# Optimization experiments

Measured on AMD Instinct MI355X. Metric: run time of the kernel, lower is better.

Reference implementation:

```python
import jax, jax.numpy as jnp
import numpy as np

A = 81          # agents / zones (9x9 grid)
DMAX = 5        # max neighborhood size (self + 4-neighbors)
NGLOB = 48      # global obs block width
HID = 128
B = 16384
LN_EPS = 1e-12  # tf.contrib.layers.layer_norm epsilon
BN_EPS = 1e-3   # tf.contrib.layers.batch_norm epsilon
NEG = -1e30


def _grid_adjacency():
    side = 9
    idx = np.zeros((A, DMAX), np.int32)
    mask = np.zeros((A, DMAX), bool)
    for i in range(A):
        r, c = divmod(i, side)
        nb = [i]
        for dr, dc in ((-1, 0), (1, 0), (0, -1), (0, 1)):
            rr, cc = r + dr, c + dc
            if 0 <= rr < side and 0 <= cc < side:
                nb.append(rr * side + cc)
        idx[i, :len(nb)] = nb
        mask[i, :len(nb)] = True
    return jnp.asarray(idx), jnp.asarray(mask)


def setup_inputs() -> dict:
    key = jax.random.key(0)
    ks = jax.random.split(key, 8)
    neigh_idx, neigh_mask = _grid_adjacency()
    in_dim = 2 * DMAX + NGLOB  # padded local obs width (58)
    s = 0.05
    return {
        "obs": jax.random.normal(ks[0], (B, 210), jnp.float32),
        "neigh_idx": neigh_idx,
        "neigh_mask": neigh_mask,
        "W1": jax.random.normal(ks[1], (A, in_dim, HID), jnp.float32) * s,
        "b1": jnp.zeros((A, HID), jnp.float32),
        "ln1_g": jnp.ones((A, HID), jnp.float32),
        "ln1_b": jnp.zeros((A, HID), jnp.float32),
        "bn1_b": jnp.zeros((A, HID), jnp.float32),
        "W2": jax.random.normal(ks[2], (A, HID, HID), jnp.float32) * s,
        "b2": jnp.zeros((A, HID), jnp.float32),
        "ln2_g": jnp.ones((A, HID), jnp.float32),
        "ln2_b": jnp.zeros((A, HID), jnp.float32),
        "bn2_b": jnp.zeros((A, HID), jnp.float32),
        "Wout": jax.random.normal(ks[3], (A, HID, DMAX), jnp.float32) * s,
        "bout": jnp.zeros((A, DMAX), jnp.float32),
    }


def _layer_norm(x, g, b):
    mu = jnp.mean(x, axis=-1, keepdims=True)
    var = jnp.mean(jnp.square(x - mu), axis=-1, keepdims=True)
    return (x - mu) * jax.lax.rsqrt(var + LN_EPS) * g[:, None, :] + b[:, None, :]


def _batch_norm(x, beta):
    # training-mode batch norm over the batch axis (axis=1), center only (scale=False)
    mu = jnp.mean(x, axis=1, keepdims=True)
    var = jnp.mean(jnp.square(x - mu), axis=1, keepdims=True)
    return (x - mu) * jax.lax.rsqrt(var + BN_EPS) + beta[:, None, :]


def reference(obs, neigh_idx, neigh_mask, W1, b1, ln1_g, ln1_b, bn1_b,
              W2, b2, ln2_g, ln2_b, bn2_b, Wout, bout):
    m = neigh_mask[:, None, :].astype(obs.dtype)          # [A,1,DMAX]
    g1 = obs[:, NGLOB + neigh_idx].transpose(1, 0, 2)      # [A,B,DMAX] zone block 1
    g2 = obs[:, NGLOB + 81 + neigh_idx].transpose(1, 0, 2)  # [A,B,DMAX] zone block 2
    glob = jnp.broadcast_to(obs[None, :, :NGLOB], (A, obs.shape[0], NGLOB))
    x = jnp.concatenate([g1 * m, g2 * m, glob], axis=-1)   # [A,B,58] (padded slots zeroed)

    h = jnp.einsum('abi,aio->abo', x, W1) + b1[:, None, :]
    h = jax.nn.relu(_batch_norm(_layer_norm(h, ln1_g, ln1_b), bn1_b))
    h = jnp.einsum('abi,aio->abo', h, W2) + b2[:, None, :]
    h = jax.nn.relu(_batch_norm(_layer_norm(h, ln2_g, ln2_b), bn2_b))

    logits = jnp.einsum('abi,aid->abd', h, Wout) + bout[:, None, :]  # [A,B,DMAX]
    logits = jnp.where(neigh_mask[:, None, :], logits, NEG)
    p = jax.nn.softmax(logits, axis=-1) * m                # masked softmax over valid neighbors

    oh = jax.nn.one_hot(neigh_idx, A, dtype=p.dtype)       # [A,DMAX,81] scatter map
    out = jnp.einsum('abd,adn->abn', p, oh)                # scatter into fixed 81-vector
    return out.transpose(1, 0, 2)                          # [B,A,81]
```

## Files before the change

kernel.cpp:

```cpp
#include <hip/hip_runtime.h>
#include <stdint.h>
#include <stddef.h>

#define N_AG 81

typedef __bf16 bf16x8 __attribute__((ext_vector_type(8)));
typedef float f32x4 __attribute__((ext_vector_type(4)));
typedef uint32_t u32v4 __attribute__((ext_vector_type(4)));
typedef uint32_t u32v2 __attribute__((ext_vector_type(2)));

#define PB 0
#define PG 128
#define PBT 256

#define SWZ(row, off) ((uint32_t)(off) ^ (((uint32_t)(row) & 7u) << 4))

__device__ __forceinline__ unsigned short b2u(__bf16 h) {
  return __builtin_bit_cast(unsigned short, h);
}

__device__ __forceinline__ f32x4 f4z() { f32x4 v; v[0]=0.f; v[1]=0.f; v[2]=0.f; v[3]=0.f; return v; }

__device__ __forceinline__ bf16x8 ld_frag(const uint8_t* p) {
  u32v4 v = *(const u32v4*)p;
  return __builtin_bit_cast(bf16x8, v);
}

__device__ __forceinline__ f32x4 mfma16(bf16x8 a, bf16x8 b, f32x4 c) {
  return __builtin_amdgcn_mfma_f32_16x16x32_bf16(a, b, c, 0, 0, 0);
}

__device__ __forceinline__ uint8_t* yslot(float* out, int b, int a) {
  size_t base = (size_t)b * 26244 + (size_t)a * 324;
  uint32_t pad = (uint32_t)(64 - (base & 63)) & 63u;
  return (uint8_t*)out + base + pad;
}

__device__ __forceinline__ float wave16_sum(float v) {
  v += __builtin_bit_cast(float, __builtin_amdgcn_update_dpp(0, __builtin_bit_cast(int, v), 0xB1, 0xF, 0xF, true));
  v += __builtin_bit_cast(float, __builtin_amdgcn_update_dpp(0, __builtin_bit_cast(int, v), 0x4E, 0xF, 0xF, true));
  v += __builtin_bit_cast(float, __builtin_amdgcn_update_dpp(0, __builtin_bit_cast(int, v), 0x141, 0xF, 0xF, true));
  v += __builtin_bit_cast(float, __builtin_amdgcn_update_dpp(0, __builtin_bit_cast(int, v), 0x140, 0xF, 0xF, true));
  return v;
}

__device__ __forceinline__ bf16x8 mk_frag(const unsigned short (&us)[8]) {
  u32v4 pk;
  pk[0] = (uint32_t)us[0] | ((uint32_t)us[1] << 16);
  pk[1] = (uint32_t)us[2] | ((uint32_t)us[3] << 16);
  pk[2] = (uint32_t)us[4] | ((uint32_t)us[5] << 16);
  pk[3] = (uint32_t)us[6] | ((uint32_t)us[7] << 16);
  return __builtin_bit_cast(bf16x8, pk);
}

__device__ __forceinline__ bf16x8 bn_frag(u32v4 yv, const f32x4 (&cf)[4]) {
  bf16x8 r;
  #pragma unroll
  for (int j = 0; j < 8; ++j) {
    uint32_t us = (j & 1) ? (yv[j >> 1] >> 16) : (yv[j >> 1] & 0xffffu);
    float f = __builtin_bit_cast(float, us << 16);
    float h = fmaf(f, cf[j >> 1][(j & 1) * 2], cf[j >> 1][(j & 1) * 2 + 1]);
    r[j] = (__bf16)fmaxf(h, 0.f);
  }
  return r;
}

__device__ __forceinline__ void bias_ln(f32x4 (&acc)[8][2], const float* s_par, int g) {
  #pragma unroll
  for (int nf = 0; nf < 2; ++nf) {
    float s = 0.f, qs = 0.f;
    #pragma unroll
    for (int mf = 0; mf < 8; ++mf) {
      #pragma unroll
      for (int rg = 0; rg < 4; ++rg) {
        float tv = acc[mf][nf][rg] + s_par[PB + 16 * mf + 4 * g + rg];
        acc[mf][nf][rg] = tv;
        s += tv;
        qs = fmaf(tv, tv, qs);
      }
    }
    s += __shfl_xor(s, 16);  s += __shfl_xor(s, 32);
    qs += __shfl_xor(qs, 16); qs += __shfl_xor(qs, 32);
    float mu = s * (1.f / 128.f);
    float var = qs * (1.f / 128.f) - mu * mu;
    float rstd = rsqrtf(var + 1e-12f);
    #pragma unroll
    for (int mf = 0; mf < 8; ++mf) {
      #pragma unroll
      for (int rg = 0; rg < 4; ++rg) {
        int o = 16 * mf + 4 * g + rg;
        acc[mf][nf][rg] = (acc[mf][nf][rg] - mu) * rstd * s_par[PG + o] + s_par[PBT + o];
      }
    }
  }
}

__device__ __forceinline__ void stats_lds(const f32x4 (&acc)[8][2],
                                          float (&s_red)[2][4][128],
                                          int wv, int g, int q) {
  #pragma unroll
  for (int mf = 0; mf < 8; ++mf) {
    #pragma unroll
    for (int rg = 0; rg < 4; ++rg) {
      float a0v = acc[mf][0][rg], a1v = acc[mf][1][rg];
      float s = a0v + a1v;
      float qq = fmaf(a0v, a0v, a1v * a1v);
      s = wave16_sum(s);
      qq = wave16_sum(qq);
      if (q == 0) {
        int o = 16 * mf + 4 * g + rg;
        s_red[0][wv][o] += s;
        s_red[1][wv][o] += qq;
      }
    }
  }
}

__device__ __forceinline__ void pack_lds(const f32x4 (&acc)[8][2], uint8_t* s_y,
                                         int wv, int g, int q) {
  #pragma unroll
  for (int nf = 0; nf < 2; ++nf) {
    uint32_t row = 32 * wv + 16 * nf + q;
    #pragma unroll
    for (int mf = 0; mf < 8; ++mf) {
      u32v2 pk;
      pk[0] = (uint32_t)b2u((__bf16)acc[mf][nf][0]) | ((uint32_t)b2u((__bf16)acc[mf][nf][1]) << 16);
      pk[1] = (uint32_t)b2u((__bf16)acc[mf][nf][2]) | ((uint32_t)b2u((__bf16)acc[mf][nf][3]) << 16);
      *(u32v2*)(s_y + row * 256 + SWZ(row, 32 * mf + 8 * g)) = pk;
    }
  }
}

__device__ __forceinline__ void burst_out(const uint8_t* s_y, float* out, int tile, int a, int t) {
  const int row = t >> 1, half = t & 1;
  uint8_t* sp = yslot(out, tile * 128 + row, a) + half * 128;
  #pragma unroll
  for (int j = 0; j < 8; ++j) {
    u32v4 v = *(const u32v4*)(s_y + row * 256 + SWZ(row, half * 128 + 16 * j));
    *(u32v4*)(sp + 16 * j) = v;
  }
}

__device__ __forceinline__ void burst_in(uint8_t* s_y, float* out, int tile, int a, int t) {
  const int row = t >> 1, half = t & 1;
  const uint8_t* sp = yslot(out, tile * 128 + row, a) + half * 128;
  #pragma unroll
  for (int j = 0; j < 8; ++j) {
    u32v4 v = *(const u32v4*)(sp + 16 * j);
    *(u32v4*)(s_y + row * 256 + SWZ(row, half * 128 + 16 * j)) = v;
  }
}

__global__ void prep_w1(const float* __restrict__ W1, uint8_t* __restrict__ w1img) {
  const int a = blockIdx.x, t = threadIdx.x;
  for (int i = t; i < 128 * 64; i += 256) {
    int o = i & 127, kk = i >> 7;
    float v;
    if (kk < 48)      v = W1[((size_t)a * 58 + (10 + kk)) * 128 + o];
    else if (kk < 58) v = W1[((size_t)a * 58 + (kk - 48)) * 128 + o];
    else              v = 0.f;
    uint32_t cb = 2u * kk;
    uint32_t phys = o * 128 + (((cb & ~15u) ^ (((uint32_t)o & 7u) << 4)) | (cb & 15u));
    *(unsigned short*)(w1img + (size_t)a * 16384 + phys) = b2u((__bf16)v);
  }
}

__global__ void prep_w2wo(const float* __restrict__ W2, const float* __restrict__ Wout,
                          uint8_t* __restrict__ w2img, uint8_t* __restrict__ woimg) {
  const int a = blockIdx.x, t = threadIdx.x;
  for (int i = t; i < 128 * 128; i += 256) {
    int o = i & 127, kk = i >> 7;
    float v = W2[((size_t)a * 128 + kk) * 128 + o];
    uint32_t cb = 2u * kk;
    uint32_t phys = o * 256 + (((cb & ~15u) ^ (((uint32_t)o & 7u) << 4)) | (cb & 15u));
    *(unsigned short*)(w2img + (size_t)a * 32768 + phys) = b2u((__bf16)v);
  }
  for (int i = t; i < 16 * 128; i += 256) {
    int k = i & 127, d = i >> 7;
    float v = (d < 5) ? Wout[((size_t)a * 128 + k) * 5 + d] : 0.f;
    uint32_t cb = 2u * k;
    uint32_t phys = d * 256 + (((cb & ~15u) ^ (((uint32_t)d & 7u) << 4)) | (cb & 15u));
    *(unsigned short*)(woimg + (size_t)a * 4096 + phys) = b2u((__bf16)v);
  }
}

__global__ void prep_obs(const float* __restrict__ obs, uint8_t* __restrict__ globimg) {
  const int row = blockIdx.x * 256 + threadIdx.x;
  if (row >= 16384) return;
  const float* orow = obs + (size_t)row * 210;
  uint8_t* dst = globimg + (size_t)row * 96;
  #pragma unroll
  for (int c = 0; c < 6; ++c) {
    u32v4 pk;
    #pragma unroll
    for (int e = 0; e < 4; ++e) {
      pk[e] = (uint32_t)b2u((__bf16)orow[8 * c + 2 * e]) |
              ((uint32_t)b2u((__bf16)orow[8 * c + 2 * e + 1]) << 16);
    }
    *(u32v4*)(dst + 16 * c) = pk;
  }
}

__global__ void prep_zimgT(const float* __restrict__ obs, unsigned short* __restrict__ zimgT) {
  __shared__ unsigned short lt[128][164];
  const int t = threadIdx.x;
  const int b0 = blockIdx.x * 128;
  for (int i = t; i < 128 * 162; i += 256) {
    int br = i / 162, n = i - 162 * br;
    lt[br][n] = b2u((__bf16)obs[(size_t)(b0 + br) * 210 + 48 + n]);
  }
  __syncthreads();
  for (int i = t; i < 162 * 128; i += 256) {
    int n = i >> 7, br = i & 127;
    zimgT[(size_t)n * 16384 + b0 + br] = lt[br][n];
  }
}

__global__ void reduce_bn(const float* __restrict__ S, const float* __restrict__ Q,
                          const float* __restrict__ beta, float2* __restrict__ bn) {
  const int a = blockIdx.x, k = threadIdx.x;
  float mu = S[a * 128 + k] * (1.f / 16384.f);
  float var = Q[a * 128 + k] * (1.f / 16384.f) - mu * mu;
  float rs = rsqrtf(var + 1e-3f);
  bn[a * 128 + k] = make_float2(rs, beta[a * 128 + k] - mu * rs);
}

__launch_bounds__(256, 2)
__global__ void pass1_kernel(const int* __restrict__ nidx,
                             const float* __restrict__ b1, const float* __restrict__ ln1g,
                             const float* __restrict__ ln1b,
                             const uint8_t* __restrict__ w1img,
                             const uint8_t* __restrict__ globimg,
                             const unsigned short* __restrict__ zimgT,
                             float* __restrict__ statS, float* __restrict__ statQ,
                             float* __restrict__ out) {
  __shared__ __align__(16) uint8_t s_w1[16384];
  __shared__ __align__(16) uint8_t s_y[32768];
  __shared__ float s_par[384];
  __shared__ float s_red[2][4][128];

  const int t = threadIdx.x;
  const int wv = t >> 6, l = t & 63, g = l >> 4, q = l & 15;
  const int a = blockIdx.x % N_AG;
  const int sub = blockIdx.x / N_AG;

  const int r9 = a / 9, c9 = a - 9 * r9;
  const int deg = 1 + (r9 > 0) + (r9 < 8) + (c9 > 0) + (c9 < 8);
  int nid[5];
  #pragma unroll
  for (int d = 0; d < 5; ++d) nid[d] = __builtin_amdgcn_readfirstlane(nidx[a * 5 + d]);

  const uint8_t* w1src = w1img + (size_t)a * 16384;
  #pragma unroll
  for (int i = 0; i < 4; ++i) ((u32v4*)s_w1)[t + 256 * i] = ((const u32v4*)w1src)[t + 256 * i];
  if (t < 128) {
    s_par[PB + t] = b1[a * 128 + t];
    s_par[PG + t] = ln1g[a * 128 + t];
    s_par[PBT + t] = ln1b[a * 128 + t];
  }
  #pragma unroll
  for (int i = 0; i < 4; ++i) ((float*)s_red)[t + 256 * i] = 0.f;
  __syncthreads();

  for (int tt = 0; tt < 4; ++tt) {
    const int tile = sub * 4 + tt;

    bf16x8 bfr[2][2];
    #pragma unroll
    for (int ks = 0; ks < 2; ++ks) {
      #pragma unroll
      for (int nf = 0; nf < 2; ++nf) {
        const int brow = tile * 128 + 32 * wv + 16 * nf + q;
        if (ks == 1 && g >= 2) {
          unsigned short us[8];
          if (g == 2) {
            #pragma unroll
            for (int e = 0; e < 5; ++e)
              us[e] = (e < deg) ? zimgT[(size_t)nid[e] * 16384 + brow] : (unsigned short)0;
            #pragma unroll
            for (int e = 0; e < 3; ++e)
              us[5 + e] = (e < deg) ? zimgT[(size_t)(81 + nid[e]) * 16384 + brow] : (unsigned short)0;
          } else {
            us[0] = (3 < deg) ? zimgT[(size_t)(81 + nid[3]) * 16384 + brow] : (unsigned short)0;
            us[1] = (4 < deg) ? zimgT[(size_t)(81 + nid[4]) * 16384 + brow] : (unsigned short)0;
            #pragma unroll
            for (int e = 2; e < 8; ++e) us[e] = 0;
          }
          bfr[ks][nf] = mk_frag(us);
        } else {
          bfr[ks][nf] = *(const bf16x8*)(globimg + (size_t)brow * 96 + (32 * ks + 8 * g) * 2);
        }
      }
    }

    f32x4 acc[8][2];
    #pragma unroll
    for (int mf = 0; mf < 8; ++mf) { acc[mf][0] = f4z(); acc[mf][1] = f4z(); }
    #pragma unroll
    for (int ks = 0; ks < 2; ++ks) {
      #pragma unroll
      for (int mf = 0; mf < 8; ++mf) {
        uint32_t r = 16 * mf + q;
        uint32_t cb = ((uint32_t)(64 * ks + 16 * g)) ^ ((r & 7u) << 4);
        bf16x8 af = ld_frag(s_w1 + r * 128 + cb);
        acc[mf][0] = mfma16(af, bfr[ks][0], acc[mf][0]);
        acc[mf][1] = mfma16(af, bfr[ks][1], acc[mf][1]);
      }
    }

    bias_ln(acc, s_par, g);
    stats_lds(acc, s_red, wv, g, q);
    pack_lds(acc, s_y, wv, g, q);
    __syncthreads();
    burst_out(s_y, out, tile, a, t);
    __syncthreads();
  }

  if (t < 128) {
    float S = s_red[0][0][t] + s_red[0][1][t] + s_red[0][2][t] + s_red[0][3][t];
    float Q = s_red[1][0][t] + s_red[1][1][t] + s_red[1][2][t] + s_red[1][3][t];
    atomicAdd(statS + a * 128 + t, S);
    atomicAdd(statQ + a * 128 + t, Q);
  }
}

__launch_bounds__(256, 2)
__global__ void pass2_kernel(const float* __restrict__ b2, const float* __restrict__ ln2g,
                             const float* __restrict__ ln2b,
                             const uint8_t* __restrict__ w2img,
                             const float2* __restrict__ bn1,
                             float* __restrict__ statS, float* __restrict__ statQ,
                             float* __restrict__ out) {
  __shared__ __align__(16) uint8_t s_w2[32768];
  __shared__ __align__(16) uint8_t s_y[32768];
  __shared__ float s_par[384];
  __shared__ __align__(16) float2 s_bnc[128];
  __shared__ float s_red[2][4][128];

  const int t = threadIdx.x;
  const int wv = t >> 6, l = t & 63, g = l >> 4, q = l & 15;
  const int a = blockIdx.x % N_AG;
  const int sub = blockIdx.x / N_AG;

  const uint8_t* w2src = w2img + (size_t)a * 32768;
  #pragma unroll
  for (int i = 0; i < 8; ++i) ((u32v4*)s_w2)[t + 256 * i] = ((const u32v4*)w2src)[t + 256 * i];
  if (t < 128) {
    s_par[PB + t] = b2[a * 128 + t];
    s_par[PG + t] = ln2g[a * 128 + t];
    s_par[PBT + t] = ln2b[a * 128 + t];
    s_bnc[t] = bn1[a * 128 + t];
  }
  #pragma unroll
  for (int i = 0; i < 4; ++i) ((float*)s_red)[t + 256 * i] = 0.f;
  __syncthreads();

  for (int tt = 0; tt < 4; ++tt) {
    const int tile = sub * 4 + tt;

    burst_in(s_y, out, tile, a, t);
    __syncthreads();

    f32x4 acc[8][2];
    #pragma unroll
    for (int mf = 0; mf < 8; ++mf) { acc[mf][0] = f4z(); acc[mf][1] = f4z(); }

    #pragma unroll
    for (int ks2 = 0; ks2 < 4; ++ks2) {
      const int k0 = 32 * ks2 + 8 * g;
      f32x4 cf[4];
      #pragma unroll
      for (int i = 0; i < 4; ++i)
        cf[i] = *(const f32x4*)((const uint8_t*)s_bnc + k0 * 8 + 16 * i);
      bf16x8 bfr[2];
      #pragma unroll
      for (int nf = 0; nf < 2; ++nf) {
        uint32_t row = 32 * wv + 16 * nf + q;
        u32v4 yv = *(const u32v4*)(s_y + row * 256 + SWZ(row, 64 * ks2 + 16 * g));
        bfr[nf] = bn_frag(yv, cf);
      }
      #pragma unroll
      for (int mf = 0; mf < 8; ++mf) {
        uint32_t r = 16 * mf + q;
        uint32_t cb = ((uint32_t)(64 * ks2 + 16 * g)) ^ ((r & 7u) << 4);
        bf16x8 af = ld_frag(s_w2 + r * 256 + cb);
        acc[mf][0] = mfma16(af, bfr[0], acc[mf][0]);
        acc[mf][1] = mfma16(af, bfr[1], acc[mf][1]);
      }
    }

    bias_ln(acc, s_par, g);
    stats_lds(acc, s_red, wv, g, q);
    __syncthreads();
    pack_lds(acc, s_y, wv, g, q);
    __syncthreads();
    burst_out(s_y, out, tile, a, t);
    __syncthreads();
  }

  if (t < 128) {
    float S = s_red[0][0][t] + s_red[0][1][t] + s_red[0][2][t] + s_red[0][3][t];
    float Q = s_red[1][0][t] + s_red[1][1][t] + s_red[1][2][t] + s_red[1][3][t];
    atomicAdd(statS + a * 128 + t, S);
    atomicAdd(statQ + a * 128 + t, Q);
  }
}

__launch_bounds__(256, 3)
__global__ void pass3_kernel(const int* __restrict__ nidx, const float* __restrict__ boutp,
                             const uint8_t* __restrict__ woimg,
                             const float2* __restrict__ bn2,
                             float* __restrict__ out) {
  __shared__ __align__(16) uint8_t s_buf[43008];
  __shared__ __align__(16) uint8_t s_wo[4096];
  __shared__ __align__(16) float2 s_bnc[128];
  __shared__ float s_bout[16];

  uint8_t* s_y = s_buf;
  float* s_out = (float*)s_buf;

  const int t = threadIdx.x;
  const int wv = t >> 6, l = t & 63, g = l >> 4, q = l & 15;
  const int a = blockIdx.x % N_AG;
  const int sub = blockIdx.x / N_AG;

  const int r9 = a / 9, c9 = a - 9 * r9;
  const int deg = 1 + (r9 > 0) + (r9 < 8) + (c9 > 0) + (c9 < 8);
  int nid[5];
  #pragma unroll
  for (int d = 0; d < 5; ++d) nid[d] = __builtin_amdgcn_readfirstlane(nidx[a * 5 + d]);

  ((u32v4*)s_wo)[t] = ((const u32v4*)(woimg + (size_t)a * 4096))[t];
  if (t < 128) s_bnc[t] = bn2[a * 128 + t];
  if (t < 16) s_bout[t] = (t < 5) ? boutp[a * 5 + t] : 0.f;
  __syncthreads();

  bf16x8 afr[4];
  #pragma unroll
  for (int ks2 = 0; ks2 < 4; ++ks2) {
    uint32_t cb = ((uint32_t)(64 * ks2 + 16 * g)) ^ (((uint32_t)q & 7u) << 4);
    afr[ks2] = ld_frag(s_wo + q * 256 + cb);
  }

  for (int tt = 0; tt < 4; ++tt) {
    const int tile = sub * 4 + tt;

    burst_in(s_y, out, tile, a, t);
    __syncthreads();

    f32x4 accd[2];
    accd[0] = f4z(); accd[1] = f4z();

    #pragma unroll
    for (int ks2 = 0; ks2 < 4; ++ks2) {
      const int k0 = 32 * ks2 + 8 * g;
      f32x4 cf[4];
      #pragma unroll
      for (int i = 0; i < 4; ++i)
        cf[i] = *(const f32x4*)((const uint8_t*)s_bnc + k0 * 8 + 16 * i);
      #pragma unroll
      for (int nf = 0; nf < 2; ++nf) {
        uint32_t row = 32 * wv + 16 * nf + q;
        u32v4 yv = *(const u32v4*)(s_y + row * 256 + SWZ(row, 64 * ks2 + 16 * g));
        accd[nf] = mfma16(afr[ks2], bn_frag(yv, cf), accd[nf]);
      }
    }

    #pragma unroll
    for (int nf = 0; nf < 2; ++nf) {
      #pragma unroll
      for (int rg = 0; rg < 4; ++rg) accd[nf][rg] += s_bout[4 * g + rg];
    }
    float d4[2];
    d4[0] = __shfl_xor(accd[0][0], 16);
    d4[1] = __shfl_xor(accd[1][0], 16);

    float p[2][5];
    #pragma unroll
    for (int nf = 0; nf < 2; ++nf) {
      float v[5] = {accd[nf][0], accd[nf][1], accd[nf][2], accd[nf][3], d4[nf]};
      float mx = v[0];
      #pragma unroll
      for (int d = 1; d < 5; ++d)
        if (d < deg) mx = fmaxf(mx, v[d]);
      float den = 0.f;
      #pragma unroll
      for (int d = 0; d < 5; ++d) {
        float e = (d < deg) ? __expf(v[d] - mx) : 0.f;
        p[nf][d] = e;
        den += e;
      }
      float inv = 1.f / den;
      #pragma unroll
      for (int d = 0; d < 5; ++d) p[nf][d] *= inv;
    }

    float p5[5];
    #pragma unroll
    for (int d = 0; d < 5; ++d) {
      float pr = __shfl_xor(p[1][d], 32);
      p5[d] = (g == 0) ? p[0][d] : pr;
    }

    __syncthreads();
    #pragma unroll
    for (int i = 0; i < 11; ++i) {
      int idx = t + 256 * i;
      if (idx < 2688) {
        u32v4 z; z[0] = 0u; z[1] = 0u; z[2] = 0u; z[3] = 0u;
        ((u32v4*)s_out)[idx] = z;
      }
    }
    __syncthreads();
    if (g == 0 || g == 2) {
      const int row = 32 * wv + ((g == 2) ? 16 : 0) + q;
      #pragma unroll
      for (int d = 0; d < 5; ++d)
        if (d < deg) s_out[row * 84 + nid[d]] = p5[d];
    }
    __syncthreads();
    const size_t obase = (size_t)(tile * 128) * 6561 + (size_t)a * 81;
    for (int i = t; i < 128 * 81; i += 256) {
      int r = i / 81;
      int n = i - r * 81;
      out[obase + (size_t)r * 6561 + n] = s_out[r * 84 + n];
    }
    __syncthreads();
  }
}

extern "C" void kernel_launch(void* const* d_in, const int* in_sizes, int n_in,
                              void* d_out, int out_size, void* d_ws, size_t ws_size,
                              hipStream_t stream) {
  (void)in_sizes; (void)n_in; (void)out_size; (void)ws_size;
  const float* obs = (const float*)d_in[0];
  const int* nidx = (const int*)d_in[1];
  const float* W1 = (const float*)d_in[3];
  const float* b1 = (const float*)d_in[4];
  const float* ln1g = (const float*)d_in[5];
  const float* ln1b = (const float*)d_in[6];
  const float* bnb1 = (const float*)d_in[7];
  const float* W2 = (const float*)d_in[8];
  const float* b2 = (const float*)d_in[9];
  const float* ln2g = (const float*)d_in[10];
  const float* ln2b = (const float*)d_in[11];
  const float* bnb2 = (const float*)d_in[12];
  const float* Wout = (const float*)d_in[13];
  const float* bout = (const float*)d_in[14];
  float* out = (float*)d_out;
  uint8_t* ws = (uint8_t*)d_ws;

  uint8_t* w1img   = ws;
  uint8_t* globimg = ws + 1327104;
  uint8_t* regionA = ws + 2899968;
  unsigned short* zimgT = (unsigned short*)regionA;
  uint8_t* w2img = regionA;
  uint8_t* woimg = regionA + 2654208;
  float* statS = (float*)(ws + 8208384);
  float* statQ = (float*)(ws + 8249856);
  float2* bn1 = (float2*)(ws + 8291328);
  float2* bn2 = (float2*)(ws + 8374272);

  prep_w1<<<N_AG, 256, 0, stream>>>(W1, w1img);
  prep_obs<<<64, 256, 0, stream>>>(obs, globimg);
  prep_zimgT<<<128, 256, 0, stream>>>(obs, zimgT);
  hipMemsetAsync(statS, 0, 2 * 41472, stream);

  pass1_kernel<<<N_AG * 32, 256, 0, stream>>>(nidx, b1, ln1g, ln1b, w1img, globimg, zimgT,
                                              statS, statQ, out);
  reduce_bn<<<N_AG, 128, 0, stream>>>(statS, statQ, bnb1, bn1);

  prep_w2wo<<<N_AG, 256, 0, stream>>>(W2, Wout, w2img, woimg);
  hipMemsetAsync(statS, 0, 2 * 41472, stream);

  pass2_kernel<<<N_AG * 32, 256, 0, stream>>>(b2, ln2g, ln2b, w2img, bn1,
                                              statS, statQ, out);
  reduce_bn<<<N_AG, 128, 0, stream>>>(statS, statQ, bnb2, bn2);

  pass3_kernel<<<N_AG * 32, 256, 0, stream>>>(nidx, bout, woimg, bn2, out);
}
```

Baseline: 755.0 us.

## Remap blocks per XCD and drop block barriers via wave-local LDS bands

Adds a block-index remap that places consecutive agent/tile work items on the same XCD, so that chiplet's L2 can share per-agent weights. It also removes several __syncthreads calls around the LDS staging steps, relying on each wave touching only its own 32 rows. The pass3 scatter-and-store is restructured so each wave zeroes, fills and writes out its own band of the output buffer without block-wide barriers. If burst_in, burst_out or pack_lds actually cross wave boundaries, the removed barriers introduce a race.

```diff
diff --git a/kernel.cpp b/kernel.cpp
--- a/kernel.cpp
+++ b/kernel.cpp
@@ -28,6 +28,12 @@
 
 __device__ __forceinline__ f32x4 mfma16(bf16x8 a, bf16x8 b, f32x4 c) {
   return __builtin_amdgcn_mfma_f32_16x16x32_bf16(a, b, c, 0, 0, 0);
+}
+
+__device__ __forceinline__ void work_id(int bid, int& a, int& sub) {
+  int w = (bid & 7) * 324 + (bid >> 3);
+  a = w % N_AG;
+  sub = w / N_AG;
 }
 
 __device__ __forceinline__ uint8_t* yslot(float* out, int b, int a) {
@@ -241,8 +247,8 @@
 
   const int t = threadIdx.x;
   const int wv = t >> 6, l = t & 63, g = l >> 4, q = l & 15;
-  const int a = blockIdx.x % N_AG;
-  const int sub = blockIdx.x / N_AG;
+  int a, sub;
+  work_id(blockIdx.x, a, sub);
 
   const int r9 = a / 9, c9 = a - 9 * r9;
   const int deg = 1 + (r9 > 0) + (r9 < 8) + (c9 > 0) + (c9 < 8);
@@ -311,7 +317,6 @@
     bias_ln(acc, s_par, g);
     stats_lds(acc, s_red, wv, g, q);
     pack_lds(acc, s_y, wv, g, q);
-    __syncthreads();
     burst_out(s_y, out, tile, a, t);
     __syncthreads();
   }
@@ -339,8 +344,8 @@
 
   const int t = threadIdx.x;
   const int wv = t >> 6, l = t & 63, g = l >> 4, q = l & 15;
-  const int a = blockIdx.x % N_AG;
-  const int sub = blockIdx.x / N_AG;
+  int a, sub;
+  work_id(blockIdx.x, a, sub);
 
   const uint8_t* w2src = w2img + (size_t)a * 32768;
   #pragma unroll
@@ -359,7 +364,6 @@
     const int tile = sub * 4 + tt;
 
     burst_in(s_y, out, tile, a, t);
-    __syncthreads();
 
     f32x4 acc[8][2];
     #pragma unroll
@@ -391,9 +395,7 @@
 
     bias_ln(acc, s_par, g);
     stats_lds(acc, s_red, wv, g, q);
-    __syncthreads();
     pack_lds(acc, s_y, wv, g, q);
-    __syncthreads();
     burst_out(s_y, out, tile, a, t);
     __syncthreads();
   }
@@ -421,8 +423,8 @@
 
   const int t = threadIdx.x;
   const int wv = t >> 6, l = t & 63, g = l >> 4, q = l & 15;
-  const int a = blockIdx.x % N_AG;
-  const int sub = blockIdx.x / N_AG;
+  int a, sub;
+  work_id(blockIdx.x, a, sub);
 
   const int r9 = a / 9, c9 = a - 9 * r9;
   const int deg = 1 + (r9 > 0) + (r9 < 8) + (c9 > 0) + (c9 < 8);
@@ -446,7 +448,6 @@
     const int tile = sub * 4 + tt;
 
     burst_in(s_y, out, tile, a, t);
-    __syncthreads();
 
     f32x4 accd[2];
     accd[0] = f4z(); accd[1] = f4z();
@@ -503,28 +504,28 @@
     }
 
     __syncthreads();
-    #pragma unroll
-    for (int i = 0; i < 11; ++i) {
-      int idx = t + 256 * i;
-      if (idx < 2688) {
+
+    {
+      uint8_t* band = (uint8_t*)s_out + (size_t)wv * 10752;
+      for (int i = l; i < 672; i += 64) {
         u32v4 z; z[0] = 0u; z[1] = 0u; z[2] = 0u; z[3] = 0u;
-        ((u32v4*)s_out)[idx] = z;
-      }
-    }
-    __syncthreads();
-    if (g == 0 || g == 2) {
-      const int row = 32 * wv + ((g == 2) ? 16 : 0) + q;
-      #pragma unroll
-      for (int d = 0; d < 5; ++d)
-        if (d < deg) s_out[row * 84 + nid[d]] = p5[d];
-    }
-    __syncthreads();
-    const size_t obase = (size_t)(tile * 128) * 6561 + (size_t)a * 81;
-    for (int i = t; i < 128 * 81; i += 256) {
-      int r = i / 81;
-      int n = i - r * 81;
-      out[obase + (size_t)r * 6561 + n] = s_out[r * 84 + n];
-    }
+        *(u32v4*)(band + (size_t)i * 16) = z;
+      }
+      if (g == 0 || g == 2) {
+        const int row = 32 * wv + ((g == 2) ? 16 : 0) + q;
+        #pragma unroll
+        for (int d = 0; d < 5; ++d)
+          if (d < deg) s_out[row * 84 + nid[d]] = p5[d];
+      }
+      const size_t obase = (size_t)(tile * 128) * 6561 + (size_t)a * 81;
+      for (int i = l; i < 32 * 81; i += 64) {
+        int rr = i / 81;
+        int n = i - rr * 81;
+        int row = 32 * wv + rr;
+        out[obase + (size_t)row * 6561 + n] = s_out[row * 84 + n];
+      }
+    }
+
     __syncthreads();
   }
 }
```

Measured after the change: 757.2 us. About the same (+0.3%).
